# Kernel tuning notes

Measured on AMD Instinct MI355X. Metric: run time of the kernel, lower is better.

## Reference

```python
import jax, jax.numpy as jnp
import numpy as np

N = 50000   # nodes
E = 640000  # edges
IN = 128    # input feature dim (== H*C so every layer has a residual)
H = 4       # heads
C = 32      # out channels per head
L = 3       # layers
D = H * C   # 128, per-layer output width
NEG_SLOPE = 0.2
LN_EPS = 1e-5


def setup_inputs() -> dict:
    key = jax.random.key(0)
    ks = jax.random.split(key, 6)
    s = 0.1  # keep activations well-scaled
    x = jax.random.normal(ks[0], (N, IN), dtype=jnp.float32)
    edge_index = jax.random.randint(ks[1], (2, E), 0, N)
    Wl = jax.random.normal(ks[2], (L, IN, D), dtype=jnp.float32) * s
    bl = jnp.zeros((L, D), dtype=jnp.float32)
    Wr = jax.random.normal(ks[3], (L, IN, D), dtype=jnp.float32) * s
    br = jnp.zeros((L, D), dtype=jnp.float32)
    att = jax.random.normal(ks[4], (L, H, C), dtype=jnp.float32) * s
    bias = jnp.zeros((L, D), dtype=jnp.float32)
    gamma = jnp.ones((L, D), dtype=jnp.float32)
    beta = jnp.zeros((L, D), dtype=jnp.float32)
    return {"x": x, "edge_index": edge_index, "Wl": Wl, "bl": bl,
            "Wr": Wr, "br": br, "att": att, "bias": bias,
            "gamma": gamma, "beta": beta}


def _gatv2_layer(x, src, dst, Wl, bl, Wr, br, att, bias):
    # GATv2Conv (concat heads, eval mode so attention dropout is identity)
    xl = (x @ Wl + bl).reshape(N, H, C)  # source transform
    xr = (x @ Wr + br).reshape(N, H, C)  # target transform
    # edge-wise gather: message along edge j->i uses xl[j] + xr[i]
    e = jax.nn.leaky_relu(xl[src] + xr[dst], NEG_SLOPE)      # [E,H,C]
    logit = jnp.einsum('ehc,hc->eh', e, att)                  # [E,H]
    # segment softmax over incoming edges of each target node
    m = jax.ops.segment_max(logit, dst, num_segments=N)       # [N,H]
    a = jnp.exp(logit - m[dst])
    denom = jax.ops.segment_sum(a, dst, num_segments=N)       # [N,H]
    a = a / (denom[dst] + 1e-16)
    # scatter-aggregate weighted source messages
    out = jax.ops.segment_sum(a[:, :, None] * xl[src], dst, num_segments=N)
    return out.reshape(N, D) + bias


def _layer_norm(h, g, b):
    mu = jnp.mean(h, axis=-1, keepdims=True)
    var = jnp.mean((h - mu) ** 2, axis=-1, keepdims=True)
    return (h - mu) * jax.lax.rsqrt(var + LN_EPS) * g + b


def reference(x, edge_index, Wl, bl, Wr, br, att, bias, gamma, beta):
    src, dst = edge_index[0], edge_index[1]
    out = x
    for l in range(L):  # small fixed layer count
        h = jax.nn.relu(_gatv2_layer(out, src, dst, Wl[l], bl[l], Wr[l], br[l], att[l], bias[l]))
        h = _layer_norm(h, gamma[l], beta[l])
        out = h + out  # in_dim == hidden*heads, so residual at every layer
    return out
```

## Files before the change

### kernel.cpp

```cpp
#include <hip/hip_runtime.h>
#include <hip/hip_bf16.h>
#include <math.h>

#define N_NODES 50000
#define N_EDGES 640000
#define DIM 128
#define NLAYER 3
#define LN_EPS 1e-5f
#define LOG2E 1.44269504088896f
#define NSCAN 49
#define NG 391
#define SCATB 2500

#if __has_builtin(__builtin_amdgcn_exp2f)
#define EXP2(x) __builtin_amdgcn_exp2f(x)
#else
#define EXP2(x) exp2f(x)
#endif

typedef __attribute__((ext_vector_type(8))) short bf16x8;
typedef __attribute__((ext_vector_type(4))) float f32x4;

__device__ inline ushort f2b(float f) {
    __hip_bfloat16 h = __float2bfloat16(f);
    return *reinterpret_cast<ushort*>(&h);
}
__device__ inline float bf_lo(unsigned u) { return __uint_as_float(u << 16); }
__device__ inline float bf_hi(unsigned u) { return __uint_as_float(u & 0xffff0000u); }
__device__ inline float lr(float t) { return fmaf(0.4f, fabsf(t), 0.6f * t); }
__device__ inline unsigned pack2(float a, float b) {
    return (unsigned)f2b(a) | ((unsigned)f2b(b) << 16);
}
__device__ inline int cw_of(int w) { return (w & 15) + 32 * (w >> 4); }

template<int CTRL>
__device__ inline float dppadd(float v) {
    int m = __builtin_amdgcn_update_dpp(0, __float_as_int(v), CTRL, 0xF, 0xF, true);
    return v + __int_as_float(m);
}
__device__ inline float reduce16(float v) {
    v = dppadd<0x124>(v);
    v = dppadd<0x128>(v);
    v = dppadd<0xB1>(v);
    v = dppadd<0x4E>(v);
    return v;
}


__global__ __launch_bounds__(256) void zerofill(int4* __restrict__ p, int n4) {
    int i = blockIdx.x * 256 + threadIdx.x;
    if (i < n4) p[i] = make_int4(0, 0, 0, 0);
}


__global__ __launch_bounds__(256) void fusedinit(
    const float* __restrict__ x, unsigned* __restrict__ curb,
    const float* __restrict__ Wl, const float* __restrict__ Wr, ushort* __restrict__ Wt,
    const int* __restrict__ dst, int* __restrict__ deg,
    const float* __restrict__ att, const float* __restrict__ bias,
    const float* __restrict__ gamma, const float* __restrict__ beta,
    float2* __restrict__ params)
{
    int b = blockIdx.x, t = threadIdx.x;
    if (b < 12500) {
        int i = b * 256 + t;
        int node = i >> 6, w = i & 63;
        int c = cw_of(w);
        curb[i] = pack2(x[node * DIM + c], x[node * DIM + c + 16]);
    } else if (b < 12884) {
        int i = (b - 12500) * 256 + t;
        if (i < NLAYER * 2 * DIM * DIM) {
            int p = i & 127, n = (i >> 7) & 127, mat = (i >> 14) & 1, l = i >> 15;
            int c = cw_of(p >> 1) + (p & 1) * 16;
            const float* W = mat ? Wr : Wl;
            Wt[i] = f2b(W[l * DIM * DIM + c * DIM + n]);
        }
    } else if (b < 15384) {
        int e = (b - 12884) * 256 + t;
        atomicAdd(&deg[dst[e]], 1);
    } else {
        int i = t;
        if (i < NLAYER * 64) {
            int l = i >> 6, w = i & 63;
            int c = cw_of(w);
            const float* A = att + l * DIM;
            const float* B = bias + l * DIM;
            const float* G = gamma + l * DIM;
            const float* E = beta + l * DIM;
            params[l * 256 + w]       = make_float2(A[c] * LOG2E, A[c + 16] * LOG2E);
            params[l * 256 + 64 + w]  = make_float2(B[c], B[c + 16]);
            params[l * 256 + 128 + w] = make_float2(G[c], G[c + 16]);
            params[l * 256 + 192 + w] = make_float2(E[c], E[c + 16]);
        }
    }
}


__global__ __launch_bounds__(1024) void scan1(const int* __restrict__ deg,
                                              int* __restrict__ rowptr,
                                              int* __restrict__ bsum,
                                              int* __restrict__ blockhist) {
    __shared__ int sd[1024];
    __shared__ int lh[256];
    int t = threadIdx.x;
    int idx = blockIdx.x * 1024 + t;
    if (t < 256) lh[t] = 0;
    __syncthreads();
    int v = (idx < N_NODES) ? deg[idx] : 0;
    if (idx < N_NODES) atomicAdd(&lh[v < 255 ? v : 255], 1);
    sd[t] = v;
    __syncthreads();
    for (int off = 1; off < 1024; off <<= 1) {
        int add = (t >= off) ? sd[t - off] : 0;
        __syncthreads();
        sd[t] += add;
        __syncthreads();
    }
    if (idx < N_NODES) rowptr[idx + 1] = sd[t];
    if (t == 1023) bsum[blockIdx.x] = sd[1023];
    if (t < 256) blockhist[blockIdx.x * 256 + t] = lh[t];
}

__global__ __launch_bounds__(1024) void midscan(const int* __restrict__ bsum,
                                                int* __restrict__ bcarry,
                                                const int* __restrict__ blockhist,
                                                int* __restrict__ bboff) {
    __shared__ int sh[256];
    int t = threadIdx.x;
    if (t < 256) {
        int tot = 0;
        for (int b = 0; b < NSCAN; ++b) tot += blockhist[b * 256 + t];
        sh[t] = tot;
    }
    __syncthreads();
    for (int off = 1; off < 256; off <<= 1) {
        int add = 0;
        if (t < 256 && t >= off) add = sh[t - off];
        __syncthreads();
        if (t < 256) sh[t] += add;
        __syncthreads();
    }
    if (t < 256) {
        int run = sh[255] - sh[t];
        for (int b = 0; b < NSCAN; ++b) {
            bboff[b * 256 + t] = run;
            run += blockhist[b * 256 + t];
        }
    }
    if (t == 0) {
        int c = 0;
        for (int b = 0; b < NSCAN; ++b) { bcarry[b] = c; c += bsum[b]; }
    }
}

__global__ __launch_bounds__(1024) void scan2(int* __restrict__ rowptr,
                                              const int* __restrict__ bcarry,
                                              const int* __restrict__ deg,
                                              const int* __restrict__ bboff,
                                              int* __restrict__ order) {
    __shared__ int lh[256];
    int t = threadIdx.x;
    int idx = blockIdx.x * 1024 + t;
    if (t < 256) lh[t] = 0;
    __syncthreads();
    int carry = bcarry[blockIdx.x];
    if (idx == 0) rowptr[0] = 0;
    if (idx < N_NODES) {
        rowptr[idx + 1] += carry;
        int d = deg[idx];
        int bin = d < 255 ? d : 255;
        int rank = atomicAdd(&lh[bin], 1);
        order[bboff[blockIdx.x * 256 + bin] + rank] = idx;
    }
}


__global__ __launch_bounds__(256) void gemm_sc(
    const ushort* __restrict__ A,
    const ushort* __restrict__ Wt_l,
    const float* __restrict__ bl, const float* __restrict__ br,
    unsigned* __restrict__ xlb, unsigned* __restrict__ xrb,
    int do_scat,
    const int* __restrict__ src, const int* __restrict__ dst,
    const int* __restrict__ rowptr, int* __restrict__ cnt,
    int* __restrict__ esrc,
    const int* __restrict__ order, const int* __restrict__ deg,
    int4* __restrict__ slotinfo)
{
    __shared__ char ldsA[32768];
    __shared__ char ldsB[32768];
    int b = blockIdx.x, t = threadIdx.x;
    if (do_scat) {
        if (b < SCATB) {
            int e = b * 256 + t;
            int d = dst[e];
            int pos = rowptr[d] + atomicAdd(&cnt[d], 1);
            esrc[pos] = src[e] << 8;
            if (e < N_NODES) {
                int nd = order[e];
                int r0 = rowptr[nd];
                slotinfo[e] = make_int4(nd, r0, r0 + deg[nd], 0);
            }
            return;
        }
        b -= SCATB;
    }

    int mat = b >= NG;
    int rowbase = (mat ? b - NG : b) * 128;

    const char* Ab = (const char*)A + (size_t)rowbase * 256;
    const char* Bb = (const char*)(Wt_l + (size_t)mat * DIM * DIM);
    #pragma unroll
    for (int i = 0; i < 8; ++i) {
        int o = (i * 256 + t) * 16;
        int row = o >> 8, ch = (o >> 4) & 15;
        int sw = row * 256 + ((ch ^ (row & 7)) << 4);
        *(uint4*)&ldsA[sw] = *(const uint4*)(Ab + o);
        *(uint4*)&ldsB[sw] = *(const uint4*)(Bb + o);
    }
    __syncthreads();

    int wid = t >> 6, lane = t & 63;
    int wr = wid >> 1, wc = wid & 1;
    int fr = lane & 15, kg = lane >> 4;

    f32x4 acc[4][4];
    #pragma unroll
    for (int mf = 0; mf < 4; ++mf)
        #pragma unroll
        for (int nf = 0; nf < 4; ++nf)
            acc[mf][nf] = (f32x4){0.f, 0.f, 0.f, 0.f};

    #pragma unroll
    for (int kf = 0; kf < 4; ++kf) {
        int c = kf * 4 + kg;
        bf16x8 af[4], bfr[4];
        #pragma unroll
        for (int mf = 0; mf < 4; ++mf) {
            int rl = wr * 64 + mf * 16 + fr;
            af[mf] = *(const bf16x8*)&ldsA[rl * 256 + ((c ^ (rl & 7)) << 4)];
        }
        #pragma unroll
        for (int nf = 0; nf < 4; ++nf) {
            int nl = wc * 64 + nf * 16 + fr;
            bfr[nf] = *(const bf16x8*)&ldsB[nl * 256 + ((c ^ (nl & 7)) << 4)];
        }
        #pragma unroll
        for (int mf = 0; mf < 4; ++mf)
            #pragma unroll
            for (int nf = 0; nf < 4; ++nf)
                acc[mf][nf] = __builtin_amdgcn_mfma_f32_16x16x32_bf16(
                    af[mf], bfr[nf], acc[mf][nf], 0, 0, 0);
    }
    __syncthreads();

    const float* bias = mat ? br : bl;
    int col = fr;
    int r4 = kg;
    float bb[4];
    #pragma unroll
    for (int nf = 0; nf < 4; ++nf) bb[nf] = bias[wc * 64 + nf * 16 + col];

    unsigned* ldsO = (unsigned*)ldsA;
    #pragma unroll
    for (int mf = 0; mf < 4; ++mf) {
        #pragma unroll
        for (int pj = 0; pj < 2; ++pj) {
            int w = col + 32 * wc + 16 * pj;
            #pragma unroll
            for (int r = 0; r < 4; ++r) {
                int rl = wr * 64 + mf * 16 + r4 * 4 + r;
                ldsO[rl * 64 + w] =
                    pack2(acc[mf][2 * pj][r] + bb[2 * pj],
                          acc[mf][2 * pj + 1][r] + bb[2 * pj + 1]);
            }
        }
    }
    __syncthreads();

    unsigned* out = mat ? xrb : xlb;
    char* ob = (char*)out + (size_t)rowbase * 256;
    #pragma unroll
    for (int i = 0; i < 8; ++i) {
        int o = (i * 256 + t) * 16;
        int row = rowbase + (o >> 8);
        if (row < N_NODES)
            *(uint4*)(ob + o) = *(const uint4*)&ldsA[o];
    }
}


__device__ inline void gather8(const char* __restrict__ xb, int laneoff,
                               const int j[8], unsigned u[8]) {
    #pragma unroll
    for (int i = 0; i < 8; ++i)
        u[i] = *(const unsigned*)(xb + j[i] + laneoff);
}

__device__ inline void compute8(const unsigned u[8], float ax, float ay,
                                float xrx, float xry,
                                float& s, float& ox, float& oy) {
    #pragma unroll
    for (int i = 0; i < 8; ++i) {
        float vx = bf_lo(u[i]), vy = bf_hi(u[i]);
        float p = lr(vx + xrx) * ax + lr(vy + xry) * ay;
        p = reduce16(p);
        float w = EXP2(p);
        s += w; ox = fmaf(w, vx, ox); oy = fmaf(w, vy, oy);
    }
}

__device__ inline void computeT(const unsigned u[8], float ax, float ay,
                                float xrx, float xry,
                                float& s, float& ox, float& oy, int rem) {
    #pragma unroll
    for (int i = 0; i < 8; ++i) {
        if (i < rem) {
            float vx = bf_lo(u[i]), vy = bf_hi(u[i]);
            float p = lr(vx + xrx) * ax + lr(vy + xry) * ay;
            p = reduce16(p);
            float w = EXP2(p);
            s += w; ox = fmaf(w, vx, ox); oy = fmaf(w, vy, oy);
        }
    }
}

__global__ __launch_bounds__(256) void agg_kernel(
    const unsigned* __restrict__ xlb2, const unsigned* __restrict__ xrb2,
    const int* __restrict__ esrc, const int4* __restrict__ slotinfo,
    const float2* __restrict__ P4,
    unsigned* __restrict__ curb, float* __restrict__ outf, int last)
{
    int slot = blockIdx.x * 4 + (threadIdx.x >> 6);
    int lane = threadIdx.x & 63;
    int4 si = slotinfo[slot];
    int node = __builtin_amdgcn_readfirstlane(si.x);
    int e0   = __builtin_amdgcn_readfirstlane(si.y);
    int e1   = __builtin_amdgcn_readfirstlane(si.z);

    unsigned xru = xrb2[node * 64 + lane];
    float2 att2 = P4[lane];
    float2 b2   = P4[64 + lane];
    float2 g2   = P4[128 + lane];
    float2 be2  = P4[192 + lane];
    unsigned old = curb[node * 64 + lane];
    float xrx = bf_lo(xru), xry = bf_hi(xru);

    const char* xb = (const char*)xlb2;
    int laneoff = lane << 2;

    float s = 0.f, ox = 0.f, oy = 0.f;
    int nb = (e1 - e0) >> 3;
    int rem = (e1 - e0) & 7;

    int jc[8], jn[8];
    unsigned uc[8], un[8];

    if (nb > 0) {
        #pragma unroll
        for (int i = 0; i < 8; ++i) jc[i] = esrc[e0 + i];
        gather8(xb, laneoff, jc, uc);
    }
    int ec = e0;
    for (int b = 1; b < nb; ++b) {
        int en = ec + 8;
        #pragma unroll
        for (int i = 0; i < 8; ++i) jn[i] = esrc[en + i];
        gather8(xb, laneoff, jn, un);
        compute8(uc, att2.x, att2.y, xrx, xry, s, ox, oy);
        #pragma unroll
        for (int i = 0; i < 8; ++i) uc[i] = un[i];
        ec = en;
    }
    if (nb > 0) {
        if (rem) {
            int et = ec + 8;
            #pragma unroll
            for (int i = 0; i < 8; ++i)
                jn[i] = esrc[et + (i < rem ? i : rem - 1)];
            gather8(xb, laneoff, jn, un);
            compute8(uc, att2.x, att2.y, xrx, xry, s, ox, oy);
            computeT(un, att2.x, att2.y, xrx, xry, s, ox, oy, rem);
        } else {
            compute8(uc, att2.x, att2.y, xrx, xry, s, ox, oy);
        }
    } else if (rem) {
        #pragma unroll
        for (int i = 0; i < 8; ++i)
            jc[i] = esrc[e0 + (i < rem ? i : rem - 1)];
        gather8(xb, laneoff, jc, uc);
        computeT(uc, att2.x, att2.y, xrx, xry, s, ox, oy, rem);
    }

    float inv = 1.f / (s + 1e-16f);
    float gx = fmaxf(fmaf(ox, inv, b2.x), 0.f);
    float gy = fmaxf(fmaf(oy, inv, b2.y), 0.f);

    float sum = gx + gy;
    sum = reduce16(sum);
    sum += __shfl_xor(sum, 16);
    sum += __shfl_xor(sum, 32);
    float mu = sum * (1.f / 128.f);
    float dx = gx - mu, dy = gy - mu;
    float ss = dx * dx + dy * dy;
    ss = reduce16(ss);
    ss += __shfl_xor(ss, 16);
    ss += __shfl_xor(ss, 32);
    float rstd = rsqrtf(ss * (1.f / 128.f) + LN_EPS);

    float yx = fmaf(dx * rstd, g2.x, be2.x) + bf_lo(old);
    float yy = fmaf(dy * rstd, g2.y, be2.y) + bf_hi(old);

    if (last) {
        int c = cw_of(lane);
        outf[node * DIM + c] = yx;
        outf[node * DIM + c + 16] = yy;
    } else {
        curb[node * 64 + lane] = pack2(yx, yy);
    }
}


extern "C" void kernel_launch(void* const* d_in, const int* in_sizes, int n_in,
                              void* d_out, int out_size, void* d_ws, size_t ws_size,
                              hipStream_t stream) {
    const float* x     = (const float*)d_in[0];
    const int*   ei    = (const int*)d_in[1];
    const float* Wl    = (const float*)d_in[2];
    const float* bl    = (const float*)d_in[3];
    const float* Wr    = (const float*)d_in[4];
    const float* br    = (const float*)d_in[5];
    const float* att   = (const float*)d_in[6];
    const float* bias  = (const float*)d_in[7];
    const float* gamma = (const float*)d_in[8];
    const float* beta  = (const float*)d_in[9];
    float* outf = (float*)d_out;

    char* ws = (char*)d_ws;
    size_t off = 0;
    auto alloc = [&](size_t bytes) -> void* {
        void* p = ws + off;
        off += (bytes + 255) & ~size_t(255);
        return p;
    };
    unsigned* curb = (unsigned*)alloc((size_t)N_NODES * 64 * 4);
    unsigned* xlb  = (unsigned*)alloc((size_t)N_NODES * 64 * 4);
    unsigned* xrb  = (unsigned*)alloc((size_t)N_NODES * 64 * 4);
    ushort* Wt     = (ushort*)alloc((size_t)NLAYER * 2 * DIM * DIM * 2);
    int* esrc      = (int*)alloc((size_t)N_EDGES * 4);
    int* rowptr    = (int*)alloc((size_t)(N_NODES + 1) * 4);
    int* zbase     = (int*)alloc((size_t)(2 * N_NODES + 2 * 64) * 4);
    int* deg = zbase, *cnt = zbase + N_NODES;
    int* bsum = cnt + N_NODES, *bcarry = bsum + 64;
    int* blockhist = (int*)alloc((size_t)NSCAN * 256 * 4);
    int* bboff     = (int*)alloc((size_t)NSCAN * 256 * 4);
    int* order     = (int*)alloc((size_t)N_NODES * 4);
    int4* slotinfo = (int4*)alloc((size_t)N_NODES * 16);
    float2* params = (float2*)alloc((size_t)NLAYER * 256 * sizeof(float2));

    const int* srcArr = ei;
    const int* dstArr = ei + N_EDGES;

    int n4 = (2 * N_NODES + 2 * 64) / 4;
    zerofill<<<(n4 + 255) / 256, 256, 0, stream>>>((int4*)zbase, n4);
    fusedinit<<<15385, 256, 0, stream>>>(x, curb, Wl, Wr, Wt, dstArr, deg,
                                         att, bias, gamma, beta, params);
    scan1<<<NSCAN, 1024, 0, stream>>>(deg, rowptr, bsum, blockhist);
    midscan<<<1, 1024, 0, stream>>>(bsum, bcarry, blockhist, bboff);
    scan2<<<NSCAN, 1024, 0, stream>>>(rowptr, bcarry, deg, bboff, order);

    for (int l = 0; l < NLAYER; ++l) {
        int do_scat = (l == 0) ? 1 : 0;
        int grid = 2 * NG + (do_scat ? SCATB : 0);
        gemm_sc<<<grid, 256, 0, stream>>>(
            (const ushort*)curb, Wt + (size_t)l * 2 * DIM * DIM,
            bl + (size_t)l * DIM, br + (size_t)l * DIM, xlb, xrb,
            do_scat, srcArr, dstArr, rowptr, cnt, esrc, order, deg, slotinfo);
        agg_kernel<<<12500, 256, 0, stream>>>(
            xlb, xrb, esrc, slotinfo, params + (size_t)l * 256,
            curb, outf, l == NLAYER - 1 ? 1 : 0);
    }
}
```

Before: 229.9 us.

## Halve GEMM row tile and keep weight fragments in registers

```diff
diff --git a/kernel.cpp b/kernel.cpp
--- a/kernel.cpp
+++ b/kernel.cpp
@@ -9,7 +9,7 @@
 #define LN_EPS 1e-5f
 #define LOG2E 1.44269504088896f
 #define NSCAN 49
-#define NG 391
+#define NG2 782
 #define SCATB 2500
 
 #if __has_builtin(__builtin_amdgcn_exp2f)
@@ -187,8 +187,7 @@
     const int* __restrict__ order, const int* __restrict__ deg,
     int4* __restrict__ slotinfo)
 {
-    __shared__ char ldsA[32768];
-    __shared__ char ldsB[32768];
+    __shared__ char lds[16384];
     int b = blockIdx.x, t = threadIdx.x;
     if (do_scat) {
         if (b < SCATB) {
@@ -206,28 +205,40 @@
         b -= SCATB;
     }
 
-    int mat = b >= NG;
-    int rowbase = (mat ? b - NG : b) * 128;
-
-    const char* Ab = (const char*)A + (size_t)rowbase * 256;
-    const char* Bb = (const char*)(Wt_l + (size_t)mat * DIM * DIM);
-    #pragma unroll
-    for (int i = 0; i < 8; ++i) {
-        int o = (i * 256 + t) * 16;
-        int row = o >> 8, ch = (o >> 4) & 15;
-        int sw = row * 256 + ((ch ^ (row & 7)) << 4);
-        *(uint4*)&ldsA[sw] = *(const uint4*)(Ab + o);
-        *(uint4*)&ldsB[sw] = *(const uint4*)(Bb + o);
-    }
-    __syncthreads();
+    int mat = b & 1;
+    int tile = b >> 1;
+    int rowbase = tile * 64;
 
     int wid = t >> 6, lane = t & 63;
     int wr = wid >> 1, wc = wid & 1;
     int fr = lane & 15, kg = lane >> 4;
 
-    f32x4 acc[4][4];
-    #pragma unroll
-    for (int mf = 0; mf < 4; ++mf)
+    const ushort* W = Wt_l + (size_t)mat * DIM * DIM;
+
+    bf16x8 bfr[4][4];
+    #pragma unroll
+    for (int kf = 0; kf < 4; ++kf)
+        #pragma unroll
+        for (int nf = 0; nf < 4; ++nf)
+            bfr[kf][nf] = *(const bf16x8*)(W + (size_t)(wc * 64 + nf * 16 + fr) * DIM
+                                             + kg * 8 + kf * 32);
+
+    const char* Ab = (const char*)A + (size_t)rowbase * 256;
+    uint4 sa[4];
+    #pragma unroll
+    for (int i = 0; i < 4; ++i)
+        sa[i] = *(const uint4*)(Ab + (i * 256 + t) * 16);
+    #pragma unroll
+    for (int i = 0; i < 4; ++i) {
+        int o = (i * 256 + t) * 16;
+        int row = o >> 8, ch = (o >> 4) & 15;
+        *(uint4*)&lds[row * 256 + ((ch ^ (row & 7)) << 4)] = sa[i];
+    }
+    __syncthreads();
+
+    f32x4 acc[2][4];
+    #pragma unroll
+    for (int mf = 0; mf < 2; ++mf)
         #pragma unroll
         for (int nf = 0; nf < 4; ++nf)
             acc[mf][nf] = (f32x4){0.f, 0.f, 0.f, 0.f};
@@ -235,42 +246,35 @@
     #pragma unroll
     for (int kf = 0; kf < 4; ++kf) {
         int c = kf * 4 + kg;
-        bf16x8 af[4], bfr[4];
-        #pragma unroll
-        for (int mf = 0; mf < 4; ++mf) {
-            int rl = wr * 64 + mf * 16 + fr;
-            af[mf] = *(const bf16x8*)&ldsA[rl * 256 + ((c ^ (rl & 7)) << 4)];
-        }
-        #pragma unroll
-        for (int nf = 0; nf < 4; ++nf) {
-            int nl = wc * 64 + nf * 16 + fr;
-            bfr[nf] = *(const bf16x8*)&ldsB[nl * 256 + ((c ^ (nl & 7)) << 4)];
-        }
-        #pragma unroll
-        for (int mf = 0; mf < 4; ++mf)
+        bf16x8 af[2];
+        #pragma unroll
+        for (int mf = 0; mf < 2; ++mf) {
+            int rl = wr * 32 + mf * 16 + fr;
+            af[mf] = *(const bf16x8*)&lds[rl * 256 + ((c ^ (rl & 7)) << 4)];
+        }
+        #pragma unroll
+        for (int mf = 0; mf < 2; ++mf)
             #pragma unroll
             for (int nf = 0; nf < 4; ++nf)
                 acc[mf][nf] = __builtin_amdgcn_mfma_f32_16x16x32_bf16(
-                    af[mf], bfr[nf], acc[mf][nf], 0, 0, 0);
+                    af[mf], bfr[kf][nf], acc[mf][nf], 0, 0, 0);
     }
     __syncthreads();
 
     const float* bias = mat ? br : bl;
-    int col = fr;
-    int r4 = kg;
     float bb[4];
     #pragma unroll
-    for (int nf = 0; nf < 4; ++nf) bb[nf] = bias[wc * 64 + nf * 16 + col];
-
-    unsigned* ldsO = (unsigned*)ldsA;
-    #pragma unroll
-    for (int mf = 0; mf < 4; ++mf) {
+    for (int nf = 0; nf < 4; ++nf) bb[nf] = bias[wc * 64 + nf * 16 + fr];
+
+    unsigned* ldsO = (unsigned*)lds;
+    #pragma unroll
+    for (int mf = 0; mf < 2; ++mf) {
         #pragma unroll
         for (int pj = 0; pj < 2; ++pj) {
-            int w = col + 32 * wc + 16 * pj;
+            int w = fr + 32 * wc + 16 * pj;
             #pragma unroll
             for (int r = 0; r < 4; ++r) {
-                int rl = wr * 64 + mf * 16 + r4 * 4 + r;
+                int rl = wr * 32 + mf * 16 + kg * 4 + r;
                 ldsO[rl * 64 + w] =
                     pack2(acc[mf][2 * pj][r] + bb[2 * pj],
                           acc[mf][2 * pj + 1][r] + bb[2 * pj + 1]);
@@ -282,11 +286,11 @@
     unsigned* out = mat ? xrb : xlb;
     char* ob = (char*)out + (size_t)rowbase * 256;
     #pragma unroll
-    for (int i = 0; i < 8; ++i) {
+    for (int i = 0; i < 4; ++i) {
         int o = (i * 256 + t) * 16;
         int row = rowbase + (o >> 8);
         if (row < N_NODES)
-            *(uint4*)(ob + o) = *(const uint4*)&ldsA[o];
+            *(uint4*)(ob + o) = *(const uint4*)&lds[o];
     }
 }
 
@@ -445,8 +449,8 @@
         return p;
     };
     unsigned* curb = (unsigned*)alloc((size_t)N_NODES * 64 * 4);
-    unsigned* xlb  = (unsigned*)alloc((size_t)N_NODES * 64 * 4);
-    unsigned* xrb  = (unsigned*)alloc((size_t)N_NODES * 64 * 4);
+    unsigned* xlb  = (unsigned*)alloc((size_t)N_NODES * 64 * 4 + 16384);
+    unsigned* xrb  = (unsigned*)alloc((size_t)N_NODES * 64 * 4 + 16384);
     ushort* Wt     = (ushort*)alloc((size_t)NLAYER * 2 * DIM * DIM * 2);
     int* esrc      = (int*)alloc((size_t)N_EDGES * 4);
     int* rowptr    = (int*)alloc((size_t)(N_NODES + 1) * 4);
@@ -472,7 +476,7 @@
 
     for (int l = 0; l < NLAYER; ++l) {
         int do_scat = (l == 0) ? 1 : 0;
-        int grid = 2 * NG + (do_scat ? SCATB : 0);
+        int grid = 2 * NG2 + (do_scat ? SCATB : 0);
         gemm_sc<<<grid, 256, 0, stream>>>(
             (const ushort*)curb, Wt + (size_t)l * 2 * DIM * DIM,
             bl + (size_t)l * DIM, br + (size_t)l * DIM, xlb, xrb,
```

Measured after the change: 249.6 us. 1.09x slower.
